# Kernel tuning notes

Hardware: AMD Instinct MI355X
Metric: run time of the kernel (lower is better)

## Reference

```python
import jax, jax.numpy as jnp
import numpy as np

ROWS, COLS = 8192, 8192
LENGTHS = [1, 4, 8, 16, 32, 64]   # <= 6 distinct slice lengths, per module assert
PER_LEN = 100                      # 100 slices of each length -> 600 slices, 12500 out cols


def _make_slices():
    rng = np.random.default_rng(0)
    slices = []
    for L in LENGTHS:
        starts = rng.integers(0, COLS - L, size=PER_LEN)
        for s in starts:
            slices.append((int(s), int(s) + L))
    rng.shuffle(slices)
    return np.asarray(slices, dtype=np.int64)  # [n_slices, 2]


def setup_inputs() -> dict:
    key = jax.random.key(0)
    input_tensor = jax.random.normal(key, (ROWS, COLS), dtype=jnp.float32)
    slices = jnp.asarray(_make_slices())
    return {"input_tensor": input_tensor, "slices": slices}


def reference(input_tensor, slices):
    # slices are static metadata (the torch module iterates them in Python);
    # build one flat column-gather index, then do a single fused gather.
    slices_np = np.asarray(slices)
    col_idx = np.concatenate([np.arange(s, e) for s, e in slices_np])  # [output_xnumel]
    idx = jnp.asarray(col_idx, dtype=jnp.int32)
    # output[r, p] = input[r, col_idx[p]]  == cat([input[:, s:e] for (s,e) in slices], dim=1)
    return jnp.take(input_tensor, idx, axis=1)
```

## Files before the change

kernel.cpp:

```cpp
#include <hip/hip_runtime.h>

#define ROWS 8192
#define COLS 8192

__global__ void build_idx_kernel(const int* __restrict__ slices, int n_slices,
                                 int* __restrict__ col_idx) {
    __shared__ int sh[1024];
    const int t = threadIdx.x;
    int s = 0, L = 0;
    if (t < n_slices) {
        s = slices[2 * t];
        const int e = slices[2 * t + 1];
        L = e - s;
    }
    sh[t] = L;
    __syncthreads();
    #pragma unroll
    for (int d = 1; d < 1024; d <<= 1) {
        int v = (t >= d) ? sh[t - d] : 0;
        __syncthreads();
        sh[t] += v;
        __syncthreads();
    }
    if (t < n_slices) {
        const int off = sh[t] - L;
        for (int i = 0; i < L; ++i) col_idx[off + i] = s + i;
    }
}

__global__ void gather_kernel(const float* __restrict__ in,
                              const int* __restrict__ col_idx,
                              float* __restrict__ out, int cols_out) {
    const int p = blockIdx.x * blockDim.x + threadIdx.x;
    if (p >= cols_out) return;
    const int c = col_idx[p];
    const size_t r0 = (size_t)blockIdx.y * 8;
    const float* inp = in + r0 * COLS + c;
    float* outp = out + r0 * (size_t)cols_out + p;
    #pragma unroll
    for (int k = 0; k < 8; ++k) {
        outp[(size_t)k * cols_out] = inp[(size_t)k * COLS];
    }
}

extern "C" void kernel_launch(void* const* d_in, const int* in_sizes, int n_in,
                              void* d_out, int out_size, void* d_ws, size_t ws_size,
                              hipStream_t stream) {
    const float* in = (const float*)d_in[0];
    const int* slices = (const int*)d_in[1];
    float* out = (float*)d_out;

    const int n_slices = in_sizes[1] / 2;
    const int cols_out = out_size / ROWS;

    int* col_idx = (int*)d_ws;

    build_idx_kernel<<<1, 1024, 0, stream>>>(slices, n_slices, col_idx);

    dim3 block(256, 1, 1);
    dim3 grid((cols_out + 255) / 256, ROWS / 8, 1);
    gather_kernel<<<grid, block, 0, stream>>>(in, col_idx, out, cols_out);
}
```

Measured before the change: 615.5 us.

## Vectorize gather with contiguous-quad detection and row-per-block grid

The gather kernel now gives each block one row and processes output columns in groups of four. When a group's four indices are consecutive it issues a single unaligned 4-wide load, otherwise four scalar loads, and it always writes a 4-wide store. The index-building kernel now fills col_idx with a binary search over prefix offsets from all 1024 threads, replacing the per-thread serial loop over slice lengths. The goal is fewer memory instructions, better coalescing and less load imbalance in index building; the cost is extra branch work and possible divergence on groups that span slice boundaries.

```diff
diff --git a/kernel.cpp b/kernel.cpp
--- a/kernel.cpp
+++ b/kernel.cpp
@@ -3,16 +3,22 @@
 #define ROWS 8192
 #define COLS 8192
 
+typedef float floatx4 __attribute__((ext_vector_type(4)));
+typedef floatx4 __attribute__((aligned(4))) floatx4u;
+
 __global__ void build_idx_kernel(const int* __restrict__ slices, int n_slices,
-                                 int* __restrict__ col_idx) {
+                                 int* __restrict__ col_idx, int cols_out) {
     __shared__ int sh[1024];
+    __shared__ int offs[1024];
+    __shared__ int starts[1024];
     const int t = threadIdx.x;
+
     int s = 0, L = 0;
     if (t < n_slices) {
         s = slices[2 * t];
-        const int e = slices[2 * t + 1];
-        L = e - s;
+        L = slices[2 * t + 1] - s;
     }
+    starts[t] = s;
     sh[t] = L;
     __syncthreads();
     #pragma unroll
@@ -22,25 +28,40 @@
         sh[t] += v;
         __syncthreads();
     }
-    if (t < n_slices) {
-        const int off = sh[t] - L;
-        for (int i = 0; i < L; ++i) col_idx[off + i] = s + i;
+    offs[t] = sh[t] - L;
+    __syncthreads();
+
+    for (int j = t; j < cols_out; j += 1024) {
+        int lo = 0, hi = n_slices - 1;
+        while (lo < hi) {
+            int mid = (lo + hi + 1) >> 1;
+            if (offs[mid] <= j) lo = mid; else hi = mid - 1;
+        }
+        col_idx[j] = starts[lo] + (j - offs[lo]);
     }
 }
 
 __global__ void gather_kernel(const float* __restrict__ in,
                               const int* __restrict__ col_idx,
                               float* __restrict__ out, int cols_out) {
-    const int p = blockIdx.x * blockDim.x + threadIdx.x;
-    if (p >= cols_out) return;
-    const int c = col_idx[p];
-    const size_t r0 = (size_t)blockIdx.y * 8;
-    const float* inp = in + r0 * COLS + c;
-    float* outp = out + r0 * (size_t)cols_out + p;
-    #pragma unroll
-    for (int k = 0; k < 8; ++k) {
-        outp[(size_t)k * cols_out] = inp[(size_t)k * COLS];
+    const int row = blockIdx.x;
+    const float* __restrict__ inr = in + (size_t)row * COLS;
+    float* __restrict__ outr = out + (size_t)row * cols_out;
+    const int nquads = cols_out >> 2;
+
+    for (int q = threadIdx.x; q < nquads; q += blockDim.x) {
+        const int4 c = ((const int4*)col_idx)[q];
+        floatx4 v;
+        if (c.y == c.x + 1 && c.z == c.x + 2 && c.w == c.x + 3) {
+            v = *(const floatx4u*)(inr + c.x);
+        } else {
+            v.x = inr[c.x]; v.y = inr[c.y]; v.z = inr[c.z]; v.w = inr[c.w];
+        }
+        *(floatx4*)(outr + 4 * q) = v;
     }
+    const int tail0 = nquads << 2;
+    for (int j = tail0 + threadIdx.x; j < cols_out; j += blockDim.x)
+        outr[j] = inr[col_idx[j]];
 }
 
 extern "C" void kernel_launch(void* const* d_in, const int* in_sizes, int n_in,
@@ -55,9 +76,6 @@
 
     int* col_idx = (int*)d_ws;
 
-    build_idx_kernel<<<1, 1024, 0, stream>>>(slices, n_slices, col_idx);
-
-    dim3 block(256, 1, 1);
-    dim3 grid((cols_out + 255) / 256, ROWS / 8, 1);
-    gather_kernel<<<grid, block, 0, stream>>>(in, col_idx, out, cols_out);
+    build_idx_kernel<<<1, 1024, 0, stream>>>(slices, n_slices, col_idx, cols_out);
+    gather_kernel<<<ROWS, 256, 0, stream>>>(in, col_idx, out, cols_out);
 }
```

New measurement: 680.5 us. +10.6%, slower.
